# Kernel tuning notes

Measured on AMD Instinct MI355X. Metric: run time of the kernel, lower is better.

## Reference

```python
import jax, jax.numpy as jnp
import numpy as np

B, N, D = 4, 4096, 768
SCALE = 1.0 / np.sqrt(D).astype(np.float32)


def setup_inputs() -> dict:
    key = jax.random.key(0)
    k1, k2, k3 = jax.random.split(key, 3)
    x = jax.random.normal(k1, (B, N, D), dtype=jnp.float32)
    w_qkv = jax.random.normal(k2, (D, 3 * D), dtype=jnp.float32) * (1.0 / np.sqrt(D))
    b_qkv = jnp.zeros((3 * D,), dtype=jnp.float32)
    w_out = jax.random.normal(k3, (D, D), dtype=jnp.float32) * (1.0 / np.sqrt(D))
    b_out = jnp.zeros((D,), dtype=jnp.float32)
    return {"x": x, "w_qkv": w_qkv, "b_qkv": b_qkv, "w_out": w_out, "b_out": b_out}


def reference(x, w_qkv, b_qkv, w_out, b_out):
    # fused QKV projection: [B,N,3D]
    qkv = jnp.einsum("bnd,de->bne", x, w_qkv) + b_qkv
    q, k, v = jnp.split(qkv, 3, axis=-1)          # each [B,N,D]
    # scaled dot-product attention (single head)
    scores = jnp.einsum("bnd,bmd->bnm", q, k) * SCALE  # [B,N,N]
    attn = jax.nn.softmax(scores, axis=-1)
    ctx = jnp.einsum("bnm,bmd->bnd", attn, v)          # [B,N,D]
    out = jnp.einsum("bnd,de->bne", ctx, w_out) + b_out
    return out
```

## Files before the change

### kernel.cpp

```cpp
#include <hip/hip_runtime.h>
#include <cstdint>
#include <cstddef>

#define BB 4
#define NN 4096
#define DD 768
#define EE 2304
#define MTOT 16384
static constexpr float ATT_SCALE = 0.03608439182435161f;

typedef _Float16 v8h __attribute__((ext_vector_type(8)));
typedef _Float16 v4h __attribute__((ext_vector_type(4)));
typedef float v4f __attribute__((ext_vector_type(4)));

__device__ __forceinline__ void async_copy16(void* lds, const void* gmem) {
  __builtin_amdgcn_global_load_lds(
      (const __attribute__((address_space(1))) uint32_t*)(uintptr_t)gmem,
      (__attribute__((address_space(3))) uint32_t*)(uintptr_t)lds,
      16, 0, 0);
}

enum { EPI_QKV = 0, EPI_F16 = 1, EPI_OUT = 2, EPI_PV = 3 };

template <int EPI>
__global__ __launch_bounds__(256) void gemm128(
    const _Float16* __restrict__ A, int lda, size_t zA,
    const _Float16* __restrict__ Bt, int ldb, size_t zB,
    int K,
    float* __restrict__ c_f32,
    _Float16* __restrict__ c_f16,
    int ldc, size_t zC, size_t chalf,
    const float* __restrict__ bias,
    _Float16* __restrict__ q_out,
    _Float16* __restrict__ k_out,
    _Float16* __restrict__ v_out) {
  __shared__ __align__(16) _Float16 As[128 * 64];
  __shared__ __align__(16) _Float16 Bs[128 * 64];

  const int tid = threadIdx.x;
  const int wid = tid >> 6, lane = tid & 63;
  const int wr = wid >> 1, wc = wid & 1;
  const int lq = lane >> 4, lr = lane & 15;
  const int m0 = blockIdx.x * 128, n0 = blockIdx.y * 128;
  const int z = blockIdx.z;
  int bidx, koff;
  if constexpr (EPI == EPI_PV) {
    bidx = z & 1;
    koff = (z >> 1) * K;
  } else {
    bidx = z;
    koff = 0;
  }

  const _Float16* Ab = A + (size_t)bidx * zA + (size_t)m0 * lda + koff;
  const _Float16* Bb = Bt + (size_t)bidx * zB + (size_t)n0 * ldb + koff;

  v4f acc[4][4] = {};

  for (int k0 = 0; k0 < K; k0 += 64) {
#pragma unroll
    for (int i = 0; i < 4; ++i) {
      const int c = i * 256 + tid;
      const int r = c >> 3;
      const int kc = (c & 7) ^ (r & 7);
      async_copy16(As + (size_t)c * 8, Ab + (size_t)r * lda + (k0 + kc * 8));
      async_copy16(Bs + (size_t)c * 8, Bb + (size_t)r * ldb + (k0 + kc * 8));
    }
    __syncthreads();

#pragma unroll
    for (int ks = 0; ks < 2; ++ks) {
      v8h af[4], bf[4];
#pragma unroll
      for (int t = 0; t < 4; ++t) {
        const int ra = wr * 64 + t * 16 + lr;
        const int rb = wc * 64 + t * 16 + lr;
        const int cb = ks * 4 + lq;
        af[t] = *(const v8h*)(As + ra * 64 + (((cb ^ (ra & 7)) << 3)));
        bf[t] = *(const v8h*)(Bs + rb * 64 + (((cb ^ (rb & 7)) << 3)));
      }
#pragma unroll
      for (int mt = 0; mt < 4; ++mt)
#pragma unroll
        for (int nt = 0; nt < 4; ++nt)
          acc[mt][nt] = __builtin_amdgcn_mfma_f32_16x16x32_f16(
              af[mt], bf[nt], acc[mt][nt], 0, 0, 0);
    }
    __syncthreads();
  }

  float* cf = nullptr;
  _Float16* ch = nullptr;
  if constexpr (EPI == EPI_PV)
    cf = c_f32 + (size_t)(z >> 1) * chalf + (size_t)bidx * zC;
  else if constexpr (EPI == EPI_OUT)
    cf = c_f32 + (size_t)bidx * zC;
  else if constexpr (EPI == EPI_F16)
    ch = c_f16 + (size_t)bidx * zC;

#pragma unroll
  for (int mt = 0; mt < 4; ++mt) {
#pragma unroll
    for (int nt = 0; nt < 4; ++nt) {
#pragma unroll
      for (int rg = 0; rg < 4; ++rg) {
        const int gm = m0 + wr * 64 + mt * 16 + lq * 4 + rg;
        const int gn = n0 + wc * 64 + nt * 16 + lr;
        float v = acc[mt][nt][rg];
        if constexpr (EPI == EPI_QKV) {
          v += bias[gn];
          if (gn < DD) {
            q_out[(size_t)gm * DD + gn] = (_Float16)(v * ATT_SCALE);
          } else if (gn < 2 * DD) {
            k_out[(size_t)gm * DD + (gn - DD)] = (_Float16)v;
          } else {
            v_out[(size_t)gm * DD + (gn - 2 * DD)] = (_Float16)v;
          }
        } else if constexpr (EPI == EPI_F16) {
          ch[(size_t)gm * ldc + gn] = (_Float16)v;
        } else {
          cf[(size_t)gm * ldc + gn] = (EPI == EPI_OUT) ? v + bias[gn] : v;
        }
      }
    }
  }
}

__global__ __launch_bounds__(256) void reduce_ctx(const float* __restrict__ h0,
                                                  const float* __restrict__ h1,
                                                  _Float16* __restrict__ out,
                                                  int n4) {
  int i = blockIdx.x * blockDim.x + threadIdx.x;
  if (i < n4) {
    v4f a = ((const v4f*)h0)[i];
    v4f b = ((const v4f*)h1)[i];
    v4h o;
#pragma unroll
    for (int j = 0; j < 4; ++j) o[j] = (_Float16)(a[j] + b[j]);
    ((v4h*)out)[i] = o;
  }
}

__global__ __launch_bounds__(256) void softmax_rows_f16(_Float16* __restrict__ S) {
  _Float16* row = S + (size_t)blockIdx.y * NN * NN + (size_t)blockIdx.x * NN;
  const int tid = threadIdx.x;
  const int lane = tid & 63, wid = tid >> 6;

  float f[16];
  float m = -3.0e38f;
#pragma unroll
  for (int i = 0; i < 2; ++i) {
    v8h v = ((const v8h*)row)[tid + i * 256];
#pragma unroll
    for (int j = 0; j < 8; ++j) {
      f[i * 8 + j] = (float)v[j];
      m = fmaxf(m, f[i * 8 + j]);
    }
  }
#pragma unroll
  for (int off = 32; off > 0; off >>= 1) m = fmaxf(m, __shfl_xor(m, off));
  __shared__ float redm[4], reds[4];
  if (lane == 0) redm[wid] = m;
  __syncthreads();
  m = fmaxf(fmaxf(redm[0], redm[1]), fmaxf(redm[2], redm[3]));

  float sum = 0.f;
#pragma unroll
  for (int i = 0; i < 16; ++i) {
    f[i] = __expf(f[i] - m);
    sum += f[i];
  }
#pragma unroll
  for (int off = 32; off > 0; off >>= 1) sum += __shfl_xor(sum, off);
  if (lane == 0) reds[wid] = sum;
  __syncthreads();
  sum = reds[0] + reds[1] + reds[2] + reds[3];
  const float inv = 1.0f / sum;
#pragma unroll
  for (int i = 0; i < 2; ++i) {
    v8h o;
#pragma unroll
    for (int j = 0; j < 8; ++j) o[j] = (_Float16)(f[i * 8 + j] * inv);
    ((v8h*)row)[tid + i * 256] = o;
  }
}

__global__ __launch_bounds__(256) void cvt_f16(const float* __restrict__ in,
                                               _Float16* __restrict__ out, int n4) {
  int i = blockIdx.x * blockDim.x + threadIdx.x;
  if (i < n4) {
    v4f v = ((const v4f*)in)[i];
    v4h o;
#pragma unroll
    for (int j = 0; j < 4; ++j) o[j] = (_Float16)v[j];
    ((v4h*)out)[i] = o;
  }
}

__global__ __launch_bounds__(256) void transpose_cvt(const float* __restrict__ in,
                                                     _Float16* __restrict__ out,
                                                     int R, int C) {
  __shared__ float tile[32][33];
  const int bx = blockIdx.x * 32;
  const int by = blockIdx.y * 32;
  const int tx = threadIdx.x & 31, ty = threadIdx.x >> 5;
#pragma unroll
  for (int i = 0; i < 32; i += 8)
    tile[ty + i][tx] = in[(size_t)(by + ty + i) * C + (bx + tx)];
  __syncthreads();
#pragma unroll
  for (int i = 0; i < 32; i += 8)
    out[(size_t)(bx + ty + i) * R + (by + tx)] = (_Float16)tile[tx][ty + i];
}

__global__ __launch_bounds__(256) void transpose_v(const _Float16* __restrict__ in,
                                                   _Float16* __restrict__ out) {
  __shared__ _Float16 tile[32][33];
  const int b = blockIdx.z;
  const _Float16* src = in + (size_t)b * NN * DD;
  _Float16* dst = out + (size_t)b * NN * DD;
  const int bx = blockIdx.x * 32;
  const int by = blockIdx.y * 32;
  const int tx = threadIdx.x & 31, ty = threadIdx.x >> 5;
#pragma unroll
  for (int i = 0; i < 32; i += 8)
    tile[ty + i][tx] = src[(size_t)(by + ty + i) * DD + (bx + tx)];
  __syncthreads();
#pragma unroll
  for (int i = 0; i < 32; i += 8)
    dst[(size_t)(bx + ty + i) * NN + (by + tx)] = tile[tx][ty + i];
}

extern "C" void kernel_launch(void* const* d_in, const int* in_sizes, int n_in,
                              void* d_out, int out_size, void* d_ws, size_t ws_size,
                              hipStream_t stream) {
  const float* x = (const float*)d_in[0];
  const float* w_qkv = (const float*)d_in[1];
  const float* b_qkv = (const float*)d_in[2];
  const float* w_out = (const float*)d_in[3];
  const float* b_out = (const float*)d_in[4];
  float* out = (float*)d_out;
  char* ws = (char*)d_ws;

  _Float16* xh    = (_Float16*)(ws + 0);
  _Float16* wqkvh = (_Float16*)(ws + 25165824);
  _Float16* wouth = (_Float16*)(ws + 28704768);
  _Float16* Qh    = (_Float16*)(ws + 29884416);
  _Float16* Kh    = (_Float16*)(ws + 55050240);
  _Float16* Vh    = (_Float16*)(ws + 80216064);
  _Float16* Sh    = (_Float16*)(ws + 105381888);
  _Float16* Vth   = (_Float16*)(ws + 0);
  _Float16* Ch    = (_Float16*)(ws + 80216064);

  const size_t zQK = (size_t)NN * DD;
  const size_t zS = (size_t)NN * NN;
  const size_t zCtx = (size_t)NN * DD;
  const size_t chalf = 2 * zCtx;

  cvt_f16<<<dim3((MTOT * DD / 4) / 256), 256, 0, stream>>>(x, xh, MTOT * DD / 4);
  transpose_cvt<<<dim3(EE / 32, DD / 32), 256, 0, stream>>>(w_qkv, wqkvh, DD, EE);
  transpose_cvt<<<dim3(DD / 32, DD / 32), 256, 0, stream>>>(w_out, wouth, DD, DD);

  gemm128<EPI_QKV><<<dim3(MTOT / 128, EE / 128), 256, 0, stream>>>(
      xh, DD, 0, wqkvh, DD, 0, DD, nullptr, nullptr, 0, 0, 0, b_qkv, Qh, Kh, Vh);

  transpose_v<<<dim3(DD / 32, NN / 32, BB), 256, 0, stream>>>(Vh, Vth);

  for (int c = 0; c < BB / 2; ++c) {
    const _Float16* Qc = Qh + (size_t)c * 2 * zQK;
    const _Float16* Kc = Kh + (size_t)c * 2 * zQK;
    const _Float16* Vtc = Vth + (size_t)c * 2 * zQK;
    gemm128<EPI_F16><<<dim3(NN / 128, NN / 128, 2), 256, 0, stream>>>(
        Qc, DD, zQK, Kc, DD, zQK, DD, nullptr, Sh, NN, zS, 0, nullptr, nullptr,
        nullptr, nullptr);
    softmax_rows_f16<<<dim3(NN, 2), 256, 0, stream>>>(Sh);
    gemm128<EPI_PV><<<dim3(NN / 128, DD / 128, 4), 256, 0, stream>>>(
        Sh, NN, zS, Vtc, NN, zQK, NN / 2, out, nullptr, DD, zCtx, chalf,
        nullptr, nullptr, nullptr, nullptr);
    reduce_ctx<<<dim3((int)(chalf / 4 / 256)), 256, 0, stream>>>(
        out, out + chalf, Ch + (size_t)c * 2 * zQK, (int)(chalf / 4));
  }

  gemm128<EPI_OUT><<<dim3(MTOT / 128, DD / 128), 256, 0, stream>>>(
      Ch, DD, 0, wouth, DD, 0, DD, out, nullptr, DD, 0, 0, b_out, nullptr,
      nullptr, nullptr);
}
```

Measured before the change: 576.8 us.

## Load GEMM A fragments directly from global and use wave-per-row softmax

The GEMM stops staging the A tile through LDS. Each wave now loads its A fragments straight from global memory into registers before the barrier, while B is still staged asynchronously into LDS. This cuts LDS traffic and capacity use but adds redundant global reads, since the two waves sharing a row block both fetch the same A rows. Separately, softmax gives each wave a full 4096-element row, which removes the cross-wave LDS reductions and barriers at the cost of 64 floats of registers per lane.

```diff
diff --git a/kernel.cpp b/kernel.cpp
--- a/kernel.cpp
+++ b/kernel.cpp
@@ -34,7 +34,6 @@
     _Float16* __restrict__ q_out,
     _Float16* __restrict__ k_out,
     _Float16* __restrict__ v_out) {
-  __shared__ __align__(16) _Float16 As[128 * 64];
   __shared__ __align__(16) _Float16 Bs[128 * 64];
 
   const int tid = threadIdx.x;
@@ -55,6 +54,11 @@
   const _Float16* Ab = A + (size_t)bidx * zA + (size_t)m0 * lda + koff;
   const _Float16* Bb = Bt + (size_t)bidx * zB + (size_t)n0 * ldb + koff;
 
+  const _Float16* Arow[4];
+#pragma unroll
+  for (int t = 0; t < 4; ++t)
+    Arow[t] = Ab + (size_t)(wr * 64 + t * 16 + lr) * lda + lq * 8;
+
   v4f acc[4][4] = {};
 
   for (int k0 = 0; k0 < K; k0 += 64) {
@@ -63,20 +67,23 @@
       const int c = i * 256 + tid;
       const int r = c >> 3;
       const int kc = (c & 7) ^ (r & 7);
-      async_copy16(As + (size_t)c * 8, Ab + (size_t)r * lda + (k0 + kc * 8));
       async_copy16(Bs + (size_t)c * 8, Bb + (size_t)r * ldb + (k0 + kc * 8));
     }
+    v8h af[2][4];
+#pragma unroll
+    for (int ks = 0; ks < 2; ++ks)
+#pragma unroll
+      for (int t = 0; t < 4; ++t)
+        af[ks][t] = *(const v8h*)(Arow[t] + k0 + ks * 32);
     __syncthreads();
 
 #pragma unroll
     for (int ks = 0; ks < 2; ++ks) {
-      v8h af[4], bf[4];
+      v8h bf[4];
 #pragma unroll
       for (int t = 0; t < 4; ++t) {
-        const int ra = wr * 64 + t * 16 + lr;
         const int rb = wc * 64 + t * 16 + lr;
         const int cb = ks * 4 + lq;
-        af[t] = *(const v8h*)(As + ra * 64 + (((cb ^ (ra & 7)) << 3)));
         bf[t] = *(const v8h*)(Bs + rb * 64 + (((cb ^ (rb & 7)) << 3)));
       }
 #pragma unroll
@@ -84,7 +91,7 @@
 #pragma unroll
         for (int nt = 0; nt < 4; ++nt)
           acc[mt][nt] = __builtin_amdgcn_mfma_f32_16x16x32_f16(
-              af[mt], bf[nt], acc[mt][nt], 0, 0, 0);
+              af[ks][mt], bf[nt], acc[mt][nt], 0, 0, 0);
     }
     __syncthreads();
   }
@@ -141,16 +148,16 @@
   }
 }
 
-__global__ __launch_bounds__(256) void softmax_rows_f16(_Float16* __restrict__ S) {
-  _Float16* row = S + (size_t)blockIdx.y * NN * NN + (size_t)blockIdx.x * NN;
-  const int tid = threadIdx.x;
-  const int lane = tid & 63, wid = tid >> 6;
-
-  float f[16];
+__global__ __launch_bounds__(256) void softmax_wave_f16(_Float16* __restrict__ S) {
+  const int wid = threadIdx.x >> 6, lane = threadIdx.x & 63;
+  const int row = blockIdx.x * 4 + wid;
+  _Float16* p = S + (size_t)blockIdx.y * NN * NN + (size_t)row * NN;
+
+  float f[64];
   float m = -3.0e38f;
 #pragma unroll
-  for (int i = 0; i < 2; ++i) {
-    v8h v = ((const v8h*)row)[tid + i * 256];
+  for (int i = 0; i < 8; ++i) {
+    v8h v = ((const v8h*)p)[lane + i * 64];
 #pragma unroll
     for (int j = 0; j < 8; ++j) {
       f[i * 8 + j] = (float)v[j];
@@ -159,29 +166,23 @@
   }
 #pragma unroll
   for (int off = 32; off > 0; off >>= 1) m = fmaxf(m, __shfl_xor(m, off));
-  __shared__ float redm[4], reds[4];
-  if (lane == 0) redm[wid] = m;
-  __syncthreads();
-  m = fmaxf(fmaxf(redm[0], redm[1]), fmaxf(redm[2], redm[3]));
 
   float sum = 0.f;
 #pragma unroll
-  for (int i = 0; i < 16; ++i) {
+  for (int i = 0; i < 64; ++i) {
     f[i] = __expf(f[i] - m);
     sum += f[i];
   }
 #pragma unroll
   for (int off = 32; off > 0; off >>= 1) sum += __shfl_xor(sum, off);
-  if (lane == 0) reds[wid] = sum;
-  __syncthreads();
-  sum = reds[0] + reds[1] + reds[2] + reds[3];
   const float inv = 1.0f / sum;
-#pragma unroll
-  for (int i = 0; i < 2; ++i) {
+
+#pragma unroll
+  for (int i = 0; i < 8; ++i) {
     v8h o;
 #pragma unroll
     for (int j = 0; j < 8; ++j) o[j] = (_Float16)(f[i * 8 + j] * inv);
-    ((v8h*)row)[tid + i * 256] = o;
+    ((v8h*)p)[lane + i * 64] = o;
   }
 }
 
@@ -273,7 +274,7 @@
     gemm128<EPI_F16><<<dim3(NN / 128, NN / 128, 2), 256, 0, stream>>>(
         Qc, DD, zQK, Kc, DD, zQK, DD, nullptr, Sh, NN, zS, 0, nullptr, nullptr,
         nullptr, nullptr);
-    softmax_rows_f16<<<dim3(NN, 2), 256, 0, stream>>>(Sh);
+    softmax_wave_f16<<<dim3(NN / 4, 2), 256, 0, stream>>>(Sh);
     gemm128<EPI_PV><<<dim3(NN / 128, DD / 128, 4), 256, 0, stream>>>(
         Sh, NN, zS, Vtc, NN, zQK, NN / 2, out, nullptr, DD, zCtx, chalf,
         nullptr, nullptr, nullptr, nullptr);
```

Result: slower. 861.1 us (+49.3%).
